# Performance work log

Measured on AMD Instinct MI355X. Metric: run time of the kernel, lower is better.

## Reference

```python
import jax, jax.numpy as jnp
import numpy as np

H = 64    # encoder/decoder hidden size
L = 10    # num_lags
D = 128   # input_dim (features)
OUT = 5   # out_dim
B = 8192


def lstm_cell(x, h, c, Wih, Whh, bih, bhh):
    # torch nn.LSTM gate order: i, f, g, o
    g = x @ Wih.T + bih + h @ Whh.T + bhh
    i, f, gg, o = jnp.split(g, 4, axis=-1)
    c = jax.nn.sigmoid(f) * c + jax.nn.sigmoid(i) * jnp.tanh(gg)
    h = jax.nn.sigmoid(o) * jnp.tanh(c)
    return h, c


def setup_inputs() -> dict:
    key = jax.random.key(0)
    ks = jax.random.split(key, 24)
    rn = lambda k, s, sc=0.05: jax.random.normal(k, s, jnp.float32) * sc
    return {
        "x": rn(ks[0], (B, L, D), 1.0),
        "y_hist": rn(ks[1], (B, L, OUT), 1.0),
        "h0_enc": rn(ks[2], (B, H), 0.1),
        "c0_enc": rn(ks[3], (B, H), 0.1),
        "h0_dec": rn(ks[4], (B, H), 0.1),
        "c0_dec": rn(ks[5], (B, H), 0.1),
        # encoder attention: Linear(2H+L -> 1)
        "enc_attn_w": rn(ks[6], (1, 2 * H + L)),
        "enc_attn_b": rn(ks[7], (1,)),
        # encoder LSTM
        "enc_Wih": rn(ks[8], (4 * H, D)),
        "enc_Whh": rn(ks[9], (4 * H, H)),
        "enc_bih": rn(ks[10], (4 * H,)),
        "enc_bhh": rn(ks[11], (4 * H,)),
        # decoder attention MLP: Linear(3H -> H), tanh, Linear(H -> 1)
        "dec_attn_w1": rn(ks[12], (H, 3 * H)),
        "dec_attn_b1": rn(ks[13], (H,)),
        "dec_attn_w2": rn(ks[14], (1, H)),
        "dec_attn_b2": rn(ks[15], (1,)),
        # decoder LSTM (input = out_dim)
        "dec_Wih": rn(ks[16], (4 * H, OUT)),
        "dec_Whh": rn(ks[17], (4 * H, H)),
        "dec_bih": rn(ks[18], (4 * H,)),
        "dec_bhh": rn(ks[19], (4 * H,)),
        # fc: Linear(H+OUT -> OUT)  (weight .normal_() in torch -> std 1)
        "fc_w": rn(ks[20], (OUT, H + OUT), 1.0),
        "fc_b": rn(ks[21], (OUT,)),
        # fc_out: Linear(2H -> OUT)
        "fcout_w": rn(ks[22], (OUT, 2 * H)),
        "fcout_b": rn(ks[23], (OUT,)),
    }


def reference(x, y_hist, h0_enc, c0_enc, h0_dec, c0_dec,
              enc_attn_w, enc_attn_b, enc_Wih, enc_Whh, enc_bih, enc_bhh,
              dec_attn_w1, dec_attn_b1, dec_attn_w2, dec_attn_b2,
              dec_Wih, dec_Whh, dec_bih, dec_bhh, fc_w, fc_b, fcout_w, fcout_b):
    # ---- encoder (input attention over features) ----
    # Linear([h; c; x_feat_series]) = wh.h + wc.c + wx.x_series + b
    wh, wc, wx = enc_attn_w[0, :H], enc_attn_w[0, H:2 * H], enc_attn_w[0, 2 * H:]
    score_x = jnp.einsum('bdl,l->bd', jnp.transpose(x, (0, 2, 1)), wx)  # [B, D]

    def enc_step(carry, x_t):
        h, c = carry
        scores = (h @ wh + c @ wc)[:, None] + score_x + enc_attn_b[0]   # [B, D]
        at = jax.nn.softmax(scores, axis=1)
        wi = at * x_t                                                   # [B, D]
        h, c = lstm_cell(wi, h, c, enc_Wih, enc_Whh, enc_bih, enc_bhh)
        return (h, c), h

    _, enc_seq = jax.lax.scan(enc_step, (h0_enc, c0_enc), jnp.transpose(x, (1, 0, 2)))
    x_enc = jnp.transpose(enc_seq, (1, 0, 2))                           # [B, L, H]

    # ---- decoder (temporal attention over encoded lags) ----
    W1h, W1c, W1x = dec_attn_w1[:, :H], dec_attn_w1[:, H:2 * H], dec_attn_w1[:, 2 * H:]
    pre = jnp.einsum('ble,he->blh', x_enc, W1x)                         # [B, L, H]
    w2 = dec_attn_w2[0]

    def dec_step(carry, y_t):
        h, c, _ = carry
        z = jnp.tanh(pre + (h @ W1h.T + c @ W1c.T + dec_attn_b1)[:, None, :])
        scores = z @ w2 + dec_attn_b2[0]                                # [B, L]
        at = jax.nn.softmax(scores, axis=1)
        ctx = jnp.einsum('bl,ble->be', at, x_enc)                       # [B, H]
        y_tilde = jnp.concatenate([ctx, y_t], axis=1) @ fc_w.T + fc_b   # [B, OUT]
        h, c = lstm_cell(y_tilde, h, c, dec_Wih, dec_Whh, dec_bih, dec_bhh)
        return (h, c, ctx), None

    (h, c, ctx), _ = jax.lax.scan(
        dec_step, (h0_dec, c0_dec, jnp.zeros_like(h0_dec)),
        jnp.transpose(y_hist, (1, 0, 2)))
    out = jnp.concatenate([h, ctx], axis=1) @ fcout_w.T + fcout_b       # [B, OUT]
    return out
```

## Files before the change

kernel.cpp:

```cpp
#include <hip/hip_runtime.h>

#define B_  8192
#define L_  10
#define D_  128
#define H_  64
#define OUT_ 5

typedef _Float16 h2 __attribute__((ext_vector_type(2)));
typedef _Float16 f16x8 __attribute__((ext_vector_type(8)));
typedef float f32x4 __attribute__((ext_vector_type(4)));
typedef unsigned int uint;

#define WS_ENCPK   0
#define WS_ENCB    24576
#define WS_DECY2   24832
#define WS_DECPK   26112
#define WS_DECB    34304
#define WS_W1HCP   34560
#define WS_W1XP    38656
#define WS_G       40960

__device__ __forceinline__ float sigmf(float x){ return 1.f/(1.f+__expf(-x)); }
__device__ __forceinline__ float tanhf_(float x){ return 1.f - 2.f/(1.f+__expf(2.f*x)); }
__device__ __forceinline__ uint pack_rtz(float a, float b){
  return __builtin_bit_cast(uint, __builtin_amdgcn_cvt_pkrtz(a, b));
}
__device__ __forceinline__ uint pack_rtn(float a, float b){
  h2 v; v.x = (_Float16)a; v.y = (_Float16)b;
  return __builtin_bit_cast(uint, v);
}
__device__ __forceinline__ float2 unpk(uint u){
  h2 v = __builtin_bit_cast(h2, u);
  return make_float2((float)v.x, (float)v.y);
}

union U4 { uint u[4]; uint4 q; f16x8 v; };

__global__ void prep_kernel(const float* __restrict__ encWih, const float* __restrict__ encWhh,
                            const float* __restrict__ encbih, const float* __restrict__ encbhh,
                            const float* __restrict__ decWih, const float* __restrict__ decWhh,
                            const float* __restrict__ decbih, const float* __restrict__ decbhh,
                            const float* __restrict__ w1, float* __restrict__ wsf)
{
  uint* ws = (uint*)wsf;
  int stride = gridDim.x * blockDim.x;
  int tid0 = blockIdx.x * blockDim.x + threadIdx.x;

  for (int idx = tid0; idx < 96*64; idx += stride) {
    int kp = idx >> 6, l = idx & 63;
    uint4 o; uint* op = (uint*)&o;
    #pragma unroll
    for (int q=0;q<4;++q){
      int j = q*64 + l;
      int k0 = 2*kp, k1 = 2*kp+1;
      float a = (k0 < 128) ? encWih[j*128 + k0] : encWhh[j*64 + (k0-128)];
      float b = (k1 < 128) ? encWih[j*128 + k1] : encWhh[j*64 + (k1-128)];
      op[q] = pack_rtn(a,b);
    }
    ((uint4*)(ws + WS_ENCPK))[idx] = o;
  }
  for (int idx = tid0; idx < 256; idx += stride) {
    int l = idx >> 2, q = idx & 3, j = q*64+l;
    wsf[WS_ENCB+idx] = encbih[j] + encbhh[j];
  }
  for (int idx = tid0; idx < 4*64; idx += stride) {
    int i = idx >> 6, l = idx & 63;
    uint4 o; uint* op = (uint*)&o;
    #pragma unroll
    for (int q=0;q<4;++q){
      int j = q*64 + l;
      int k0 = 2*i, k1 = 2*i+1;
      float a = (k0 < 5) ? decWih[j*5 + k0] : 0.f;
      float b = (k1 < 5) ? decWih[j*5 + k1] : 0.f;
      op[q] = pack_rtn(a,b);
    }
    ((uint4*)(ws + WS_DECY2))[idx] = o;
  }
  for (int idx = tid0; idx < 32*64; idx += stride) {
    int ep = idx >> 6, l = idx & 63;
    uint4 o; uint* op = (uint*)&o;
    #pragma unroll
    for (int q=0;q<4;++q){
      int j = q*64 + l;
      op[q] = pack_rtn(decWhh[j*64 + 2*ep], decWhh[j*64 + 2*ep+1]);
    }
    ((uint4*)(ws + WS_DECPK))[idx] = o;
  }
  for (int idx = tid0; idx < 256; idx += stride) {
    int l = idx >> 2, q = idx & 3, j = q*64+l;
    wsf[WS_DECB+idx] = decbih[j] + decbhh[j];
  }
  for (int idx = tid0; idx < 32*64; idx += stride) {
    int ep = idx >> 6, l = idx & 63;
    uint2 o;
    o.x = pack_rtn(w1[l*192 + 2*ep],      w1[l*192 + 2*ep+1]);
    o.y = pack_rtn(w1[l*192 + 64 + 2*ep], w1[l*192 + 64 + 2*ep+1]);
    ((uint2*)(ws + WS_W1HCP))[idx] = o;
  }
  for (int idx = tid0; idx < 32*64; idx += stride) {
    int ep = idx >> 6, l = idx & 63;
    ws[WS_W1XP + idx] = pack_rtn(w1[l*192 + 128 + 2*ep], w1[l*192 + 128 + 2*ep+1]);
  }
}

__global__ __launch_bounds__(256, 2) void gemmG_mfma(
    const float* __restrict__ x, const float* __restrict__ enc_attn_w,
    const float* __restrict__ ws, _Float16* __restrict__ Gh)
{
  const int tid = threadIdx.x;
  const int b0  = blockIdx.x * 16;
  const uint* wsu = (const uint*)ws;

  __shared__ _Float16 wiS[L_][16][136];

  const int l   = tid & 63;
  const int w   = tid >> 6;
  const int col = l & 15;
  const int g   = l >> 4;

  f16x8 afr[4][4];
  #pragma unroll
  for (int im=0; im<4; ++im){
    #pragma unroll
    for (int kf=0; kf<4; ++kf){
      U4 cv;
      #pragma unroll
      for (int i=0;i<4;++i){
        int kp = kf*16 + g*4 + i;
        int lsrc = im*16 + col;
        cv.u[i] = wsu[WS_ENCPK + (kp*64 + lsrc)*4 + w];
      }
      afr[im][kf] = cv.v;
    }
  }
  float bias[4][4];
  #pragma unroll
  for (int im=0; im<4; ++im)
    #pragma unroll
    for (int r=0; r<4; ++r)
      bias[im][r] = ws[WS_ENCB + (im*16 + g*4 + r)*4 + w];

  const int b  = tid >> 4;
  const int kc = tid & 15;
  const float* xb = x + (size_t)(b0+b)*(L_*D_) + kc*8;

  float wxv[L_];
  #pragma unroll
  for (int t=0;t<L_;++t) wxv[t] = enc_attn_w[2*H_ + t];

  float s[8];
  #pragma unroll
  for (int j=0;j<8;++j) s[j]=0.f;
  #pragma unroll
  for (int t=0;t<L_;++t){
    float wx = wxv[t];
    float4 x0 = *(const float4*)(xb + t*D_);
    float4 x1 = *(const float4*)(xb + t*D_ + 4);
    s[0]+=x0.x*wx; s[1]+=x0.y*wx; s[2]+=x0.z*wx; s[3]+=x0.w*wx;
    s[4]+=x1.x*wx; s[5]+=x1.y*wx; s[6]+=x1.z*wx; s[7]+=x1.w*wx;
  }
  float m = s[0];
  #pragma unroll
  for (int j=1;j<8;++j) m = fmaxf(m, s[j]);
  m = fmaxf(m, __shfl_xor(m,1));
  m = fmaxf(m, __shfl_xor(m,2));
  m = fmaxf(m, __shfl_xor(m,4));
  m = fmaxf(m, __shfl_xor(m,8));
  float at[8];
  float ss = 0.f;
  #pragma unroll
  for (int j=0;j<8;++j){ at[j] = __expf(s[j]-m); ss += at[j]; }
  ss += __shfl_xor(ss,1);
  ss += __shfl_xor(ss,2);
  ss += __shfl_xor(ss,4);
  ss += __shfl_xor(ss,8);
  float inv = 1.f/ss;
  #pragma unroll
  for (int j=0;j<8;++j) at[j] *= inv;

  #pragma unroll
  for (int t=0;t<L_;++t){
    float4 x0 = *(const float4*)(xb + t*D_);
    float4 x1 = *(const float4*)(xb + t*D_ + 4);
    uint4 o;
    o.x = pack_rtz(at[0]*x0.x, at[1]*x0.y);
    o.y = pack_rtz(at[2]*x0.z, at[3]*x0.w);
    o.z = pack_rtz(at[4]*x1.x, at[5]*x1.y);
    o.w = pack_rtz(at[6]*x1.z, at[7]*x1.w);
    *(uint4*)&wiS[t][b][kc*8] = o;
  }
  __syncthreads();

  #pragma unroll 2
  for (int t=0;t<L_;++t){
    U4 bu[4];
    #pragma unroll
    for (int kf=0;kf<4;++kf)
      bu[kf].q = *(const uint4*)&wiS[t][col][kf*32 + g*8];
    _Float16* grow = Gh + ((size_t)(b0+col)*L_ + t)*256;
    #pragma unroll
    for (int im=0;im<4;++im){
      f32x4 acc = { bias[im][0], bias[im][1], bias[im][2], bias[im][3] };
      #pragma unroll
      for (int kf=0;kf<4;++kf)
        acc = __builtin_amdgcn_mfma_f32_16x16x32_f16(afr[im][kf], bu[kf].v, acc, 0, 0, 0);
      uint2 o = make_uint2(pack_rtn(acc[0],acc[1]), pack_rtn(acc[2],acc[3]));
      *(uint2*)(grow + (4*w+im)*16 + g*4) = o;
    }
  }
}

#define SM_HXE   0
#define SM_XES   4608
#define SM_TMPF  0
#define SM_TMPG  12800
#define SM_HXD   27648
#define SM_CXD   32256
#define SM_SRED  36864
#define SM_FXE   39424
#define SM_GXE   42624
#define SM_YBS   45824
#define SM_TOTAL 49024

__global__ __launch_bounds__(256, 2) void darnn_kernel(
    const float* __restrict__ y_hist,
    const float* __restrict__ h0e, const float* __restrict__ c0e,
    const float* __restrict__ h0d, const float* __restrict__ c0d,
    const float* __restrict__ dec_attn_b1, const float* __restrict__ dec_attn_w2,
    const float* __restrict__ fc_w, const float* __restrict__ fc_b,
    const float* __restrict__ fcout_w, const float* __restrict__ fcout_b,
    const float* __restrict__ ws, const uint2* __restrict__ Gp,
    float* __restrict__ out)
{
  const int tid = threadIdx.x;
  const int l   = tid & 63;
  const int w   = tid >> 6;
  const int col = l & 15;
  const int g   = l >> 4;
  const int b0  = blockIdx.x * 16;
  const int lw  = 16*w + col;
  const int u0  = 16*w + 4*g;

  const uint* wsu = (const uint*)ws;
  const _Float16* Gh = (const _Float16*)Gp;

  __shared__ __align__(16) char smem_[SM_TOTAL];
  uint     (*hxE)[16][36] = reinterpret_cast<uint(*)[16][36]>(smem_ + SM_HXE);
  _Float16 (*xeS)[16][72] = reinterpret_cast<_Float16(*)[16][72]>(smem_ + SM_XES);
  float* tmpF = (float*)(smem_ + SM_TMPF);
  float* tmpG = (float*)(smem_ + SM_TMPG);
  uint     (*hxD)[16][36] = reinterpret_cast<uint(*)[16][36]>(smem_ + SM_HXD);
  uint     (*cxD)[16][36] = reinterpret_cast<uint(*)[16][36]>(smem_ + SM_CXD);
  float* sred = (float*)(smem_ + SM_SRED);
  float* fxeS = (float*)(smem_ + SM_FXE);
  float* gxeS = (float*)(smem_ + SM_GXE);
  float* ybS  = (float*)(smem_ + SM_YBS);

  const bool yact = (tid < 200);
  if (yact){
    float4 yreg = *(const float4*)(y_hist + (size_t)b0*50 + tid*4);
    *(float4*)(ybS + tid*4) = yreg;
  }
  float4 hd4 = *(const float4*)(h0d + (size_t)(b0+col)*64 + u0);
  float4 cd4 = *(const float4*)(c0d + (size_t)(b0+col)*64 + u0);

  f16x8 aE[4][2];
  #pragma unroll
  for (int q=0;q<4;++q)
    #pragma unroll
    for (int kf=0;kf<2;++kf){
      U4 cv;
      #pragma unroll
      for (int i=0;i<4;++i)
        cv.u[i] = wsu[WS_ENCPK + ((64 + kf*16 + g*4 + i)*64 + lw)*4 + q];
      aE[q][kf] = cv.v;
    }

  float h[4], c[4], xer[L_][4];
  {
    float4 hv = *(const float4*)(h0e + (size_t)(b0+col)*64 + u0);
    float4 cv = *(const float4*)(c0e + (size_t)(b0+col)*64 + u0);
    h[0]=hv.x; h[1]=hv.y; h[2]=hv.z; h[3]=hv.w;
    c[0]=cv.x; c[1]=cv.y; c[2]=cv.z; c[3]=cv.w;
  }
  *(uint2*)&hxE[0][col][u0>>1] = make_uint2(pack_rtz(h[0],h[1]), pack_rtz(h[2],h[3]));
  __syncthreads();

  uint2 gq[2][4];
  {
    const _Float16* g0 = Gh + ((size_t)(b0+col)*L_ + 0)*256;
    const _Float16* g1 = Gh + ((size_t)(b0+col)*L_ + 1)*256;
    #pragma unroll
    for (int q=0;q<4;++q){
      gq[0][q] = *(const uint2*)(g0 + q*64 + u0);
      gq[1][q] = *(const uint2*)(g1 + q*64 + u0);
    }
  }

  int p = 0;
  for (int t=0; t<L_; ++t){
    const int cb = t&1;
    f32x4 acc[4];
    #pragma unroll
    for (int q=0;q<4;++q){
      float2 u0f = unpk(gq[cb][q].x), u1f = unpk(gq[cb][q].y);
      acc[q][0]=u0f.x; acc[q][1]=u0f.y; acc[q][2]=u1f.x; acc[q][3]=u1f.y;
    }
    if (t+2<L_){
      const _Float16* gn = Gh + ((size_t)(b0+col)*L_ + (t+2))*256;
      #pragma unroll
      for (int q=0;q<4;++q) gq[cb][q] = *(const uint2*)(gn + q*64 + u0);
    }
    f16x8 hB[2];
    { U4 t0; t0.q = *(const uint4*)&hxE[p][col][g*4];      hB[0]=t0.v; }
    { U4 t1; t1.q = *(const uint4*)&hxE[p][col][16 + g*4]; hB[1]=t1.v; }

    #pragma unroll
    for (int q=0;q<4;++q){
      acc[q] = __builtin_amdgcn_mfma_f32_16x16x32_f16(aE[q][0], hB[0], acc[q], 0,0,0);
      acc[q] = __builtin_amdgcn_mfma_f32_16x16x32_f16(aE[q][1], hB[1], acc[q], 0,0,0);
    }
    #pragma unroll
    for (int r=0;r<4;++r){
      float ig=sigmf(acc[0][r]), fg=sigmf(acc[1][r]), gg=tanhf_(acc[2][r]), og=sigmf(acc[3][r]);
      c[r]=fg*c[r]+ig*gg;
      h[r]=og*tanhf_(c[r]);
      xer[t][r]=h[r];
    }
    uint2 hpk = make_uint2(pack_rtz(h[0],h[1]), pack_rtz(h[2],h[3]));
    *(uint2*)&xeS[t][col][u0] = hpk;
    *(uint2*)&hxE[p^1][col][u0>>1] = hpk;
    __syncthreads();
    p ^= 1;
  }

  f16x8 aX[2];
  #pragma unroll
  for (int kf=0;kf<2;++kf){
    U4 cv;
    #pragma unroll
    for (int i=0;i<4;++i) cv.u[i] = wsu[WS_W1XP + (kf*16 + g*4 + i)*64 + lw];
    aX[kf] = cv.v;
  }
  f32x4 preC[L_];
  #pragma unroll
  for (int lt=0;lt<L_;++lt){
    f32x4 a = {0.f,0.f,0.f,0.f};
    U4 bu0, bu1;
    bu0.q = *(const uint4*)&xeS[lt][col][g*8];
    bu1.q = *(const uint4*)&xeS[lt][col][32 + g*8];
    a = __builtin_amdgcn_mfma_f32_16x16x32_f16(aX[0], bu0.v, a, 0,0,0);
    a = __builtin_amdgcn_mfma_f32_16x16x32_f16(aX[1], bu1.v, a, 0,0,0);
    preC[lt] = a;
  }
  __syncthreads();

  {
    float fw1v[OUT_][4], gw1v[OUT_][4];
    #pragma unroll
    for (int o2=0;o2<OUT_;++o2)
      #pragma unroll
      for (int r=0;r<4;++r){
        fw1v[o2][r] = fc_w[o2*69 + u0 + r];
        gw1v[o2][r] = fcout_w[o2*128 + 64 + u0 + r];
      }
    #pragma unroll
    for (int lt=0;lt<L_;++lt){
      #pragma unroll
      for (int o2=0;o2<OUT_;++o2){
        float pf = fw1v[o2][0]*xer[lt][0] + fw1v[o2][1]*xer[lt][1]
                 + fw1v[o2][2]*xer[lt][2] + fw1v[o2][3]*xer[lt][3];
        float pg = gw1v[o2][0]*xer[lt][0] + gw1v[o2][1]*xer[lt][1]
                 + gw1v[o2][2]*xer[lt][2] + gw1v[o2][3]*xer[lt][3];
        pf += __shfl_xor(pf,16); pf += __shfl_xor(pf,32);
        pg += __shfl_xor(pg,16); pg += __shfl_xor(pg,32);
        if (g==0){
          tmpF[((lt*16+col)*OUT_+o2)*4 + w] = pf;
          tmpG[((lt*16+col)*OUT_+o2)*4 + w] = pg;
        }
      }
    }
  }
  __syncthreads();
  for (int idx=tid; idx<800; idx+=256){
    float4 f4 = *(const float4*)(tmpF + idx*4);
    float4 g4 = *(const float4*)(tmpG + idx*4);
    int o2 = idx % 5, rest = idx / 5;
    int b  = rest % 16, lt = rest / 16;
    fxeS[b*50 + lt*5 + o2] = f4.x+f4.y+f4.z+f4.w;
    gxeS[b*50 + lt*5 + o2] = g4.x+g4.y+g4.z+g4.w;
  }

  f16x8 aW1[4];
  #pragma unroll
  for (int kf=0;kf<4;++kf){
    U4 cv;
    #pragma unroll
    for (int i=0;i<4;++i){
      int ep = (kf&1)*16 + g*4 + i;
      cv.u[i] = wsu[WS_W1HCP + (ep*64 + lw)*2 + (kf>>1)];
    }
    aW1[kf] = cv.v;
  }
  f16x8 aGh[4][2];
  #pragma unroll
  for (int q=0;q<4;++q)
    #pragma unroll
    for (int kf=0;kf<2;++kf){
      U4 cv;
      #pragma unroll
      for (int i=0;i<4;++i)
        cv.u[i] = wsu[WS_DECPK + ((kf*16 + g*4 + i)*64 + lw)*4 + q];
      aGh[q][kf] = cv.v;
    }
  f16x8 aG0[4];
  #pragma unroll
  for (int q=0;q<4;++q){
    U4 cv;
    #pragma unroll
    for (int i=0;i<4;++i)
      cv.u[i] = (g==0) ? wsu[WS_DECY2 + (i*64 + lw)*4 + q] : 0u;
    aG0[q] = cv.v;
  }
  float4 bD[4];
  #pragma unroll
  for (int r=0;r<4;++r) bD[r] = *(const float4*)(ws + WS_DECB + (u0+r)*4);
  float4 b1v = *(const float4*)(dec_attn_b1 + u0);
  float4 w2v = *(const float4*)(dec_attn_w2 + u0);
  float fcbv[OUT_], fw2v[OUT_][OUT_];
  #pragma unroll
  for (int o2=0;o2<OUT_;++o2){
    fcbv[o2] = fc_b[o2];
    #pragma unroll
    for (int j=0;j<OUT_;++j) fw2v[o2][j] = fc_w[o2*69 + 64 + j];
  }

  h[0]=hd4.x; h[1]=hd4.y; h[2]=hd4.z; h[3]=hd4.w;
  c[0]=cd4.x; c[1]=cd4.y; c[2]=cd4.z; c[3]=cd4.w;
  *(uint2*)&hxD[0][col][u0>>1] = make_uint2(pack_rtz(h[0],h[1]), pack_rtz(h[2],h[3]));
  *(uint2*)&cxD[0][col][u0>>1] = make_uint2(pack_rtz(c[0],c[1]), pack_rtz(c[2],c[3]));
  __syncthreads();

  float at[L_];
  float inv = 0.f;
  p = 0;
  for (int t=0; t<L_; ++t){
    f16x8 hB[2], cB[2];
    { U4 t0; t0.q = *(const uint4*)&hxD[p][col][g*4];      hB[0]=t0.v; }
    { U4 t1; t1.q = *(const uint4*)&hxD[p][col][16 + g*4]; hB[1]=t1.v; }
    { U4 t2; t2.q = *(const uint4*)&cxD[p][col][g*4];      cB[0]=t2.v; }
    { U4 t3; t3.q = *(const uint4*)&cxD[p][col][16 + g*4]; cB[1]=t3.v; }

    f32x4 vb = { b1v.x, b1v.y, b1v.z, b1v.w };
    vb = __builtin_amdgcn_mfma_f32_16x16x32_f16(aW1[0], hB[0], vb, 0,0,0);
    vb = __builtin_amdgcn_mfma_f32_16x16x32_f16(aW1[1], hB[1], vb, 0,0,0);
    vb = __builtin_amdgcn_mfma_f32_16x16x32_f16(aW1[2], cB[0], vb, 0,0,0);
    vb = __builtin_amdgcn_mfma_f32_16x16x32_f16(aW1[3], cB[1], vb, 0,0,0);

    #pragma unroll
    for (int lt=0;lt<L_;++lt){
      float zp = tanhf_(preC[lt][0] + vb[0]) * w2v.x
               + tanhf_(preC[lt][1] + vb[1]) * w2v.y
               + tanhf_(preC[lt][2] + vb[2]) * w2v.z
               + tanhf_(preC[lt][3] + vb[3]) * w2v.w;
      zp += __shfl_xor(zp,16);
      zp += __shfl_xor(zp,32);
      at[lt] = zp;
    }
    if (g==0){
      #pragma unroll
      for (int lt=0;lt<L_;++lt) sred[(lt*16+col)*4 + w] = at[lt];
    }
    __syncthreads();
    #pragma unroll
    for (int lt=0;lt<L_;++lt){
      float4 s4 = *(const float4*)(sred + (lt*16+col)*4);
      at[lt] = s4.x + s4.y + s4.z + s4.w;
    }
    float mx = at[0];
    #pragma unroll
    for (int lt=1;lt<L_;++lt) mx = fmaxf(mx, at[lt]);
    float ssum = 0.f;
    #pragma unroll
    for (int lt=0;lt<L_;++lt){ at[lt] = __expf(at[lt]-mx); ssum += at[lt]; }
    inv = 1.f/ssum;

    U4 ycv; ycv.u[0]=0u; ycv.u[1]=0u; ycv.u[2]=0u; ycv.u[3]=0u;
    if (g==0){
      const float* fx = fxeS + col*50;
      const float* yb = ybS + col*50 + t*5;
      float yt[OUT_];
      #pragma unroll
      for (int o2=0;o2<OUT_;++o2){
        float s = 0.f;
        #pragma unroll
        for (int lt=0;lt<L_;++lt) s += at[lt]*fx[lt*5+o2];
        float v = s*inv + fcbv[o2];
        #pragma unroll
        for (int j=0;j<OUT_;++j) v += yb[j]*fw2v[o2][j];
        yt[o2] = v;
      }
      ycv.u[0] = pack_rtn(yt[0], yt[1]);
      ycv.u[1] = pack_rtn(yt[2], yt[3]);
      ycv.u[2] = pack_rtn(yt[4], 0.f);
    }
    f32x4 accQ[4];
    #pragma unroll
    for (int q=0;q<4;++q){
      accQ[q][0]=((const float*)&bD[0])[q];
      accQ[q][1]=((const float*)&bD[1])[q];
      accQ[q][2]=((const float*)&bD[2])[q];
      accQ[q][3]=((const float*)&bD[3])[q];
    }
    #pragma unroll
    for (int q=0;q<4;++q){
      accQ[q] = __builtin_amdgcn_mfma_f32_16x16x32_f16(aG0[q], ycv.v, accQ[q], 0,0,0);
      accQ[q] = __builtin_amdgcn_mfma_f32_16x16x32_f16(aGh[q][0], hB[0], accQ[q], 0,0,0);
      accQ[q] = __builtin_amdgcn_mfma_f32_16x16x32_f16(aGh[q][1], hB[1], accQ[q], 0,0,0);
    }
    #pragma unroll
    for (int r=0;r<4;++r){
      float ig=sigmf(accQ[0][r]), fg=sigmf(accQ[1][r]), gg=tanhf_(accQ[2][r]), og=sigmf(accQ[3][r]);
      c[r]=fg*c[r]+ig*gg;
      h[r]=og*tanhf_(c[r]);
    }
    *(uint2*)&hxD[p^1][col][u0>>1] = make_uint2(pack_rtz(h[0],h[1]), pack_rtz(h[2],h[3]));
    *(uint2*)&cxD[p^1][col][u0>>1] = make_uint2(pack_rtz(c[0],c[1]), pack_rtz(c[2],c[3]));
    __syncthreads();
    p ^= 1;
  }

  {
    float fcA[OUT_][4];
    #pragma unroll
    for (int o2=0;o2<OUT_;++o2)
      #pragma unroll
      for (int r=0;r<4;++r) fcA[o2][r] = fcout_w[o2*128 + u0 + r];
    #pragma unroll
    for (int o2=0;o2<OUT_;++o2){
      float pv = fcA[o2][0]*h[0] + fcA[o2][1]*h[1] + fcA[o2][2]*h[2] + fcA[o2][3]*h[3];
      pv += __shfl_xor(pv,16);
      pv += __shfl_xor(pv,32);
      if (g==0) sred[(o2*16+col)*4 + w] = pv;
    }
  }
  __syncthreads();
  if (w==0 && g==0){
    const float* gx = gxeS + col*50;
    #pragma unroll
    for (int o2=0;o2<OUT_;++o2){
      float4 s4 = *(const float4*)(sred + (o2*16+col)*4);
      float s = 0.f;
      #pragma unroll
      for (int lt=0;lt<L_;++lt) s += at[lt]*gx[lt*5+o2];
      out[(size_t)(b0+col)*OUT_ + o2] = s4.x+s4.y+s4.z+s4.w + s*inv + fcout_b[o2];
    }
  }
}

extern "C" void kernel_launch(void* const* d_in, const int* in_sizes, int n_in,
                              void* d_out, int out_size, void* d_ws, size_t ws_size,
                              hipStream_t stream) {
  const float* x          = (const float*)d_in[0];
  const float* y_hist     = (const float*)d_in[1];
  const float* h0_enc     = (const float*)d_in[2];
  const float* c0_enc     = (const float*)d_in[3];
  const float* h0_dec     = (const float*)d_in[4];
  const float* c0_dec     = (const float*)d_in[5];
  const float* enc_attn_w = (const float*)d_in[6];
  const float* enc_Wih    = (const float*)d_in[8];
  const float* enc_Whh    = (const float*)d_in[9];
  const float* enc_bih    = (const float*)d_in[10];
  const float* enc_bhh    = (const float*)d_in[11];
  const float* dec_attn_w1= (const float*)d_in[12];
  const float* dec_attn_b1= (const float*)d_in[13];
  const float* dec_attn_w2= (const float*)d_in[14];
  const float* dec_Wih    = (const float*)d_in[16];
  const float* dec_Whh    = (const float*)d_in[17];
  const float* dec_bih    = (const float*)d_in[18];
  const float* dec_bhh    = (const float*)d_in[19];
  const float* fc_w       = (const float*)d_in[20];
  const float* fc_b       = (const float*)d_in[21];
  const float* fcout_w    = (const float*)d_in[22];
  const float* fcout_b    = (const float*)d_in[23];
  float* ws = (float*)d_ws;
  float* out = (float*)d_out;
  uint2* Gp = (uint2*)((uint*)d_ws + WS_G);

  hipLaunchKernelGGL(prep_kernel, dim3(128), dim3(256), 0, stream,
                     enc_Wih, enc_Whh, enc_bih, enc_bhh,
                     dec_Wih, dec_Whh, dec_bih, dec_bhh,
                     dec_attn_w1, ws);
  hipLaunchKernelGGL(gemmG_mfma, dim3(B_/16), dim3(256), 0, stream,
                     x, enc_attn_w, ws, (_Float16*)Gp);
  hipLaunchKernelGGL(darnn_kernel, dim3(B_/16), dim3(256), 0, stream,
                     y_hist, h0_enc, c0_enc, h0_dec, c0_dec,
                     dec_attn_b1, dec_attn_w2,
                     fc_w, fc_b, fcout_w, fcout_b, ws, Gp, out);
}
```

Before: 253.9 us.

## Fuse encoder input-projection GEMM into recurrent kernel, keep gates in registers

Folds the separate MFMA kernel that computed the attended-input gate projections into the main recurrent kernel. The results for all 10 timesteps now stay in registers as packed fp16 (gq[L][4]) instead of being written to and re-read from a global workspace buffer. This removes one kernel launch and the roughly 42 MB global round trip of the G tensor. The cost is higher register pressure (afr, bias and gq held together under launch_bounds(256,2)), which may cause spills or lower occupancy. The GEMM A-fragments are also re-indexed so each wave computes gates for its own hidden units.

```diff
diff --git a/kernel.cpp b/kernel.cpp
--- a/kernel.cpp
+++ b/kernel.cpp
@@ -18,7 +18,6 @@
 #define WS_DECB    34304
 #define WS_W1HCP   34560
 #define WS_W1XP    38656
-#define WS_G       40960
 
 __device__ __forceinline__ float sigmf(float x){ return 1.f/(1.f+__expf(-x)); }
 __device__ __forceinline__ float tanhf_(float x){ return 1.f - 2.f/(1.f+__expf(2.f*x)); }
@@ -103,113 +102,6 @@
   }
 }
 
-__global__ __launch_bounds__(256, 2) void gemmG_mfma(
-    const float* __restrict__ x, const float* __restrict__ enc_attn_w,
-    const float* __restrict__ ws, _Float16* __restrict__ Gh)
-{
-  const int tid = threadIdx.x;
-  const int b0  = blockIdx.x * 16;
-  const uint* wsu = (const uint*)ws;
-
-  __shared__ _Float16 wiS[L_][16][136];
-
-  const int l   = tid & 63;
-  const int w   = tid >> 6;
-  const int col = l & 15;
-  const int g   = l >> 4;
-
-  f16x8 afr[4][4];
-  #pragma unroll
-  for (int im=0; im<4; ++im){
-    #pragma unroll
-    for (int kf=0; kf<4; ++kf){
-      U4 cv;
-      #pragma unroll
-      for (int i=0;i<4;++i){
-        int kp = kf*16 + g*4 + i;
-        int lsrc = im*16 + col;
-        cv.u[i] = wsu[WS_ENCPK + (kp*64 + lsrc)*4 + w];
-      }
-      afr[im][kf] = cv.v;
-    }
-  }
-  float bias[4][4];
-  #pragma unroll
-  for (int im=0; im<4; ++im)
-    #pragma unroll
-    for (int r=0; r<4; ++r)
-      bias[im][r] = ws[WS_ENCB + (im*16 + g*4 + r)*4 + w];
-
-  const int b  = tid >> 4;
-  const int kc = tid & 15;
-  const float* xb = x + (size_t)(b0+b)*(L_*D_) + kc*8;
-
-  float wxv[L_];
-  #pragma unroll
-  for (int t=0;t<L_;++t) wxv[t] = enc_attn_w[2*H_ + t];
-
-  float s[8];
-  #pragma unroll
-  for (int j=0;j<8;++j) s[j]=0.f;
-  #pragma unroll
-  for (int t=0;t<L_;++t){
-    float wx = wxv[t];
-    float4 x0 = *(const float4*)(xb + t*D_);
-    float4 x1 = *(const float4*)(xb + t*D_ + 4);
-    s[0]+=x0.x*wx; s[1]+=x0.y*wx; s[2]+=x0.z*wx; s[3]+=x0.w*wx;
-    s[4]+=x1.x*wx; s[5]+=x1.y*wx; s[6]+=x1.z*wx; s[7]+=x1.w*wx;
-  }
-  float m = s[0];
-  #pragma unroll
-  for (int j=1;j<8;++j) m = fmaxf(m, s[j]);
-  m = fmaxf(m, __shfl_xor(m,1));
-  m = fmaxf(m, __shfl_xor(m,2));
-  m = fmaxf(m, __shfl_xor(m,4));
-  m = fmaxf(m, __shfl_xor(m,8));
-  float at[8];
-  float ss = 0.f;
-  #pragma unroll
-  for (int j=0;j<8;++j){ at[j] = __expf(s[j]-m); ss += at[j]; }
-  ss += __shfl_xor(ss,1);
-  ss += __shfl_xor(ss,2);
-  ss += __shfl_xor(ss,4);
-  ss += __shfl_xor(ss,8);
-  float inv = 1.f/ss;
-  #pragma unroll
-  for (int j=0;j<8;++j) at[j] *= inv;
-
-  #pragma unroll
-  for (int t=0;t<L_;++t){
-    float4 x0 = *(const float4*)(xb + t*D_);
-    float4 x1 = *(const float4*)(xb + t*D_ + 4);
-    uint4 o;
-    o.x = pack_rtz(at[0]*x0.x, at[1]*x0.y);
-    o.y = pack_rtz(at[2]*x0.z, at[3]*x0.w);
-    o.z = pack_rtz(at[4]*x1.x, at[5]*x1.y);
-    o.w = pack_rtz(at[6]*x1.z, at[7]*x1.w);
-    *(uint4*)&wiS[t][b][kc*8] = o;
-  }
-  __syncthreads();
-
-  #pragma unroll 2
-  for (int t=0;t<L_;++t){
-    U4 bu[4];
-    #pragma unroll
-    for (int kf=0;kf<4;++kf)
-      bu[kf].q = *(const uint4*)&wiS[t][col][kf*32 + g*8];
-    _Float16* grow = Gh + ((size_t)(b0+col)*L_ + t)*256;
-    #pragma unroll
-    for (int im=0;im<4;++im){
-      f32x4 acc = { bias[im][0], bias[im][1], bias[im][2], bias[im][3] };
-      #pragma unroll
-      for (int kf=0;kf<4;++kf)
-        acc = __builtin_amdgcn_mfma_f32_16x16x32_f16(afr[im][kf], bu[kf].v, acc, 0, 0, 0);
-      uint2 o = make_uint2(pack_rtn(acc[0],acc[1]), pack_rtn(acc[2],acc[3]));
-      *(uint2*)(grow + (4*w+im)*16 + g*4) = o;
-    }
-  }
-}
-
 #define SM_HXE   0
 #define SM_XES   4608
 #define SM_TMPF  0
@@ -222,14 +114,15 @@
 #define SM_YBS   45824
 #define SM_TOTAL 49024
 
-__global__ __launch_bounds__(256, 2) void darnn_kernel(
+__global__ __launch_bounds__(256, 2) void darnn_fused(
+    const float* __restrict__ x, const float* __restrict__ enc_attn_w,
     const float* __restrict__ y_hist,
     const float* __restrict__ h0e, const float* __restrict__ c0e,
     const float* __restrict__ h0d, const float* __restrict__ c0d,
     const float* __restrict__ dec_attn_b1, const float* __restrict__ dec_attn_w2,
     const float* __restrict__ fc_w, const float* __restrict__ fc_b,
     const float* __restrict__ fcout_w, const float* __restrict__ fcout_b,
-    const float* __restrict__ ws, const uint2* __restrict__ Gp,
+    const float* __restrict__ ws,
     float* __restrict__ out)
 {
   const int tid = threadIdx.x;
@@ -242,9 +135,9 @@
   const int u0  = 16*w + 4*g;
 
   const uint* wsu = (const uint*)ws;
-  const _Float16* Gh = (const _Float16*)Gp;
 
   __shared__ __align__(16) char smem_[SM_TOTAL];
+  _Float16 (*wiS)[16][136] = reinterpret_cast<_Float16(*)[16][136]>(smem_);
   uint     (*hxE)[16][36] = reinterpret_cast<uint(*)[16][36]>(smem_ + SM_HXE);
   _Float16 (*xeS)[16][72] = reinterpret_cast<_Float16(*)[16][72]>(smem_ + SM_XES);
   float* tmpF = (float*)(smem_ + SM_TMPF);
@@ -256,13 +149,104 @@
   float* gxeS = (float*)(smem_ + SM_GXE);
   float* ybS  = (float*)(smem_ + SM_YBS);
 
-  const bool yact = (tid < 200);
-  if (yact){
+  if (tid < 200){
     float4 yreg = *(const float4*)(y_hist + (size_t)b0*50 + tid*4);
     *(float4*)(ybS + tid*4) = yreg;
   }
   float4 hd4 = *(const float4*)(h0d + (size_t)(b0+col)*64 + u0);
   float4 cd4 = *(const float4*)(c0d + (size_t)(b0+col)*64 + u0);
+  float4 he4 = *(const float4*)(h0e + (size_t)(b0+col)*64 + u0);
+  float4 ce4 = *(const float4*)(c0e + (size_t)(b0+col)*64 + u0);
+
+  f16x8 afr[4][4];
+  #pragma unroll
+  for (int im=0; im<4; ++im){
+    #pragma unroll
+    for (int kf=0; kf<4; ++kf){
+      U4 cv;
+      #pragma unroll
+      for (int i=0;i<4;++i){
+        int kp = kf*16 + g*4 + i;
+        cv.u[i] = wsu[WS_ENCPK + (kp*64 + lw)*4 + im];
+      }
+      afr[im][kf] = cv.v;
+    }
+  }
+  float bias[4][4];
+  #pragma unroll
+  for (int im=0; im<4; ++im)
+    #pragma unroll
+    for (int r=0; r<4; ++r)
+      bias[im][r] = ws[WS_ENCB + (u0 + r)*4 + im];
+
+  const int bb = tid >> 4;
+  const int kc = tid & 15;
+  const float* xb = x + (size_t)(b0+bb)*(L_*D_) + kc*8;
+
+  float wxv[L_];
+  #pragma unroll
+  for (int t=0;t<L_;++t) wxv[t] = enc_attn_w[2*H_ + t];
+
+  float s[8];
+  #pragma unroll
+  for (int j=0;j<8;++j) s[j]=0.f;
+  #pragma unroll
+  for (int t=0;t<L_;++t){
+    float wx = wxv[t];
+    float4 x0 = *(const float4*)(xb + t*D_);
+    float4 x1 = *(const float4*)(xb + t*D_ + 4);
+    s[0]+=x0.x*wx; s[1]+=x0.y*wx; s[2]+=x0.z*wx; s[3]+=x0.w*wx;
+    s[4]+=x1.x*wx; s[5]+=x1.y*wx; s[6]+=x1.z*wx; s[7]+=x1.w*wx;
+  }
+  float m = s[0];
+  #pragma unroll
+  for (int j=1;j<8;++j) m = fmaxf(m, s[j]);
+  m = fmaxf(m, __shfl_xor(m,1));
+  m = fmaxf(m, __shfl_xor(m,2));
+  m = fmaxf(m, __shfl_xor(m,4));
+  m = fmaxf(m, __shfl_xor(m,8));
+  float atw[8];
+  float ss = 0.f;
+  #pragma unroll
+  for (int j=0;j<8;++j){ atw[j] = __expf(s[j]-m); ss += atw[j]; }
+  ss += __shfl_xor(ss,1);
+  ss += __shfl_xor(ss,2);
+  ss += __shfl_xor(ss,4);
+  ss += __shfl_xor(ss,8);
+  float ainv = 1.f/ss;
+  #pragma unroll
+  for (int j=0;j<8;++j) atw[j] *= ainv;
+
+  #pragma unroll
+  for (int t=0;t<L_;++t){
+    float4 x0 = *(const float4*)(xb + t*D_);
+    float4 x1 = *(const float4*)(xb + t*D_ + 4);
+    uint4 o;
+    o.x = pack_rtz(atw[0]*x0.x, atw[1]*x0.y);
+    o.y = pack_rtz(atw[2]*x0.z, atw[3]*x0.w);
+    o.z = pack_rtz(atw[4]*x1.x, atw[5]*x1.y);
+    o.w = pack_rtz(atw[6]*x1.z, atw[7]*x1.w);
+    *(uint4*)&wiS[t][bb][kc*8] = o;
+  }
+  __syncthreads();
+
+  uint2 gq[L_][4];
+  #pragma unroll
+  for (int t=0;t<L_;++t){
+    U4 bu[4];
+    #pragma unroll
+    for (int kf=0;kf<4;++kf)
+      bu[kf].q = *(const uint4*)&wiS[t][col][kf*32 + g*8];
+    #pragma unroll
+    for (int im=0;im<4;++im){
+      f32x4 acc = { bias[im][0], bias[im][1], bias[im][2], bias[im][3] };
+      #pragma unroll
+      for (int kf=0;kf<4;++kf)
+        acc = __builtin_amdgcn_mfma_f32_16x16x32_f16(afr[im][kf], bu[kf].v, acc, 0, 0, 0);
+      gq[t][im] = make_uint2(pack_rtn(acc[0],acc[1]), pack_rtn(acc[2],acc[3]));
+    }
+  }
+  __syncthreads();
 
   f16x8 aE[4][2];
   #pragma unroll
@@ -277,39 +261,19 @@
     }
 
   float h[4], c[4], xer[L_][4];
-  {
-    float4 hv = *(const float4*)(h0e + (size_t)(b0+col)*64 + u0);
-    float4 cv = *(const float4*)(c0e + (size_t)(b0+col)*64 + u0);
-    h[0]=hv.x; h[1]=hv.y; h[2]=hv.z; h[3]=hv.w;
-    c[0]=cv.x; c[1]=cv.y; c[2]=cv.z; c[3]=cv.w;
-  }
+  h[0]=he4.x; h[1]=he4.y; h[2]=he4.z; h[3]=he4.w;
+  c[0]=ce4.x; c[1]=ce4.y; c[2]=ce4.z; c[3]=ce4.w;
   *(uint2*)&hxE[0][col][u0>>1] = make_uint2(pack_rtz(h[0],h[1]), pack_rtz(h[2],h[3]));
   __syncthreads();
 
-  uint2 gq[2][4];
-  {
-    const _Float16* g0 = Gh + ((size_t)(b0+col)*L_ + 0)*256;
-    const _Float16* g1 = Gh + ((size_t)(b0+col)*L_ + 1)*256;
-    #pragma unroll
-    for (int q=0;q<4;++q){
-      gq[0][q] = *(const uint2*)(g0 + q*64 + u0);
-      gq[1][q] = *(const uint2*)(g1 + q*64 + u0);
-    }
-  }
-
   int p = 0;
+  #pragma unroll
   for (int t=0; t<L_; ++t){
-    const int cb = t&1;
     f32x4 acc[4];
     #pragma unroll
     for (int q=0;q<4;++q){
-      float2 u0f = unpk(gq[cb][q].x), u1f = unpk(gq[cb][q].y);
+      float2 u0f = unpk(gq[t][q].x), u1f = unpk(gq[t][q].y);
       acc[q][0]=u0f.x; acc[q][1]=u0f.y; acc[q][2]=u1f.x; acc[q][3]=u1f.y;
-    }
-    if (t+2<L_){
-      const _Float16* gn = Gh + ((size_t)(b0+col)*L_ + (t+2))*256;
-      #pragma unroll
-      for (int q=0;q<4;++q) gq[cb][q] = *(const uint2*)(gn + q*64 + u0);
     }
     f16x8 hB[2];
     { U4 t0; t0.q = *(const uint4*)&hxE[p][col][g*4];      hB[0]=t0.v; }
@@ -492,10 +456,10 @@
       float yt[OUT_];
       #pragma unroll
       for (int o2=0;o2<OUT_;++o2){
-        float s = 0.f;
+        float sv = 0.f;
         #pragma unroll
-        for (int lt=0;lt<L_;++lt) s += at[lt]*fx[lt*5+o2];
-        float v = s*inv + fcbv[o2];
+        for (int lt=0;lt<L_;++lt) sv += at[lt]*fx[lt*5+o2];
+        float v = sv*inv + fcbv[o2];
         #pragma unroll
         for (int j=0;j<OUT_;++j) v += yb[j]*fw2v[o2][j];
         yt[o2] = v;
@@ -550,10 +514,10 @@
     #pragma unroll
     for (int o2=0;o2<OUT_;++o2){
       float4 s4 = *(const float4*)(sred + (o2*16+col)*4);
-      float s = 0.f;
-      #pragma unroll
-      for (int lt=0;lt<L_;++lt) s += at[lt]*gx[lt*5+o2];
-      out[(size_t)(b0+col)*OUT_ + o2] = s4.x+s4.y+s4.z+s4.w + s*inv + fcout_b[o2];
+      float sv = 0.f;
+      #pragma unroll
+      for (int lt=0;lt<L_;++lt) sv += at[lt]*gx[lt*5+o2];
+      out[(size_t)(b0+col)*OUT_ + o2] = s4.x+s4.y+s4.z+s4.w + sv*inv + fcout_b[o2];
     }
   }
 }
@@ -585,16 +549,14 @@
   const float* fcout_b    = (const float*)d_in[23];
   float* ws = (float*)d_ws;
   float* out = (float*)d_out;
-  uint2* Gp = (uint2*)((uint*)d_ws + WS_G);
 
   hipLaunchKernelGGL(prep_kernel, dim3(128), dim3(256), 0, stream,
                      enc_Wih, enc_Whh, enc_bih, enc_bhh,
                      dec_Wih, dec_Whh, dec_bih, dec_bhh,
                      dec_attn_w1, ws);
-  hipLaunchKernelGGL(gemmG_mfma, dim3(B_/16), dim3(256), 0, stream,
-                     x, enc_attn_w, ws, (_Float16*)Gp);
-  hipLaunchKernelGGL(darnn_kernel, dim3(B_/16), dim3(256), 0, stream,
-                     y_hist, h0_enc, c0_enc, h0_dec, c0_dec,
+  hipLaunchKernelGGL(darnn_fused, dim3(B_/16), dim3(256), 0, stream,
+                     x, enc_attn_w, y_hist,
+                     h0_enc, c0_enc, h0_dec, c0_dec,
                      dec_attn_b1, dec_attn_w2,
-                     fc_w, fc_b, fcout_w, fcout_b, ws, Gp, out);
+                     fc_w, fc_b, fcout_w, fcout_b, ws, out);
 }
```

Result: faster. 220.6 us (-13.1%).
